# Performance work log

Hardware: AMD Instinct MI355X
Metric: run time of the kernel (lower is better)

Reference implementation:

```python
import jax, jax.numpy as jnp
import numpy as np

B, C, T = 8, 256, 2048
REDUCED = max(C // 8, 8)  # 32


def setup_inputs() -> dict:
    key = jax.random.key(0)
    ks = jax.random.split(key, 7)
    s = 1.0 / np.sqrt(C)
    return {
        "x": jax.random.normal(ks[0], (B, C, T), dtype=jnp.float32),
        "Wq": jax.random.uniform(ks[1], (REDUCED, C), jnp.float32, -s, s),
        "bq": jax.random.uniform(ks[2], (REDUCED,), jnp.float32, -s, s),
        "Wk": jax.random.uniform(ks[3], (REDUCED, C), jnp.float32, -s, s),
        "bk": jax.random.uniform(ks[4], (REDUCED,), jnp.float32, -s, s),
        "Wv": jax.random.uniform(ks[5], (C, C), jnp.float32, -s, s),
        "bv": jax.random.uniform(ks[6], (C,), jnp.float32, -s, s),
        "gamma": jnp.zeros((1,), dtype=jnp.float32) + 0.1,  # nonzero so output depends on attention
    }


def reference(x, Wq, bq, Wk, bk, Wv, bv, gamma):
    # conv1x1 projections == per-timestep linear over channels
    q = jnp.einsum("rc,bct->btr", Wq, x) + bq            # [B, T, reduced]
    k = jnp.einsum("rc,bct->brt", Wk, x) + bk[:, None]   # [B, reduced, T]
    v = jnp.einsum("oc,bct->bto", Wv, x) + bv            # [B, T, C]
    attn = jnp.einsum("btr,brs->bts", q, k)              # [B, T, T]
    attn = jax.nn.softmax(attn, axis=-1)
    out = jnp.einsum("bts,bsc->btc", attn, v)            # [B, T, C]
    out = jnp.transpose(out, (0, 2, 1))                  # [B, C, T]
    return x + gamma * out
```

## Files before the change

### kernel.cpp

```cpp
#include <hip/hip_runtime.h>
#include <hip/hip_bf16.h>
#include <math.h>

constexpr int BB = 8;
constexpr int CC = 256;
constexpr int TT = 2048;
constexpr int RR = 32;

constexpr int ATILE = 64;
constexpr int PS = 72;

constexpr int PT  = 32;
constexpr int XS32 = 33;
constexpr int XSB  = 264;

constexpr float FIXEDM = 24.0f;

typedef short short8 __attribute__((ext_vector_type(8)));
typedef float f32x4 __attribute__((ext_vector_type(4)));
typedef unsigned short us4 __attribute__((ext_vector_type(4)));

static __device__ __forceinline__ unsigned short f2bf(float f) {
    __hip_bfloat16 h = __float2bfloat16(f);
    return *reinterpret_cast<unsigned short*>(&h);
}

__global__ __launch_bounds__(256) void wcast_kernel(
    const float* __restrict__ Wq, const float* __restrict__ Wk,
    const float* __restrict__ Wv,
    unsigned short* __restrict__ wqb, unsigned short* __restrict__ wkb,
    unsigned short* __restrict__ wvb)
{
    int g = blockIdx.x * 256 + threadIdx.x;
    const float* src; unsigned short* dst; int i4;
    if (g < 2048)       { src = Wq; dst = wqb; i4 = g; }
    else if (g < 4096)  { src = Wk; dst = wkb; i4 = g - 2048; }
    else                { src = Wv; dst = wvb; i4 = g - 4096; }
    float4 v = *(const float4*)(src + i4 * 4);
    us4 p;
    p[0] = f2bf(v.x); p[1] = f2bf(v.y); p[2] = f2bf(v.z); p[3] = f2bf(v.w);
    *(us4*)(dst + i4 * 4) = p;
}

__global__ __launch_bounds__(256, 2) void proj_kernel(
    const float* __restrict__ x,
    const unsigned short* __restrict__ wqb, const float* __restrict__ bq,
    const unsigned short* __restrict__ wkb, const float* __restrict__ bk,
    const unsigned short* __restrict__ wvb, const float* __restrict__ bv,
    unsigned short* __restrict__ qws, unsigned short* __restrict__ kws,
    unsigned short* __restrict__ vws)
{
    __shared__ float xs32[CC * XS32];
    __shared__ unsigned short xsb[PT * XSB];

    const int tid = threadIdx.x;
    const int t0  = blockIdx.x * PT;
    const int b   = blockIdx.y;
    const float* xb = x + (size_t)b * CC * TT;

    #pragma unroll
    for (int m = 0; m < 8; ++m) {
        int lin = m * 256 + tid;
        int c   = lin >> 3;
        int t4  = lin & 7;
        float4 v = *(const float4*)(xb + (size_t)c * TT + t0 + t4 * 4);
        float* d = &xs32[c * XS32 + t4 * 4];
        d[0] = v.x; d[1] = v.y; d[2] = v.z; d[3] = v.w;
    }
    __syncthreads();
    {
        int c = tid;
        #pragma unroll
        for (int t = 0; t < PT; ++t)
            xsb[t * XSB + c] = f2bf(xs32[c * XS32 + t]);
    }
    __syncthreads();

    const int lane = tid & 63;
    const int w    = __builtin_amdgcn_readfirstlane(tid >> 6);
    const int l15  = lane & 15;
    const int quad = lane >> 4;

    const unsigned short* Wt[5]; const float* bt[5]; int rl[5]; int seg[5];
    #pragma unroll
    for (int i = 0; i < 5; ++i) {
        int mt = w * 5 + i;
        if (mt < 2)      { Wt[i] = wqb; bt[i] = bq; rl[i] = mt * 16;       seg[i] = 0; }
        else if (mt < 4) { Wt[i] = wkb; bt[i] = bk; rl[i] = (mt - 2) * 16; seg[i] = 1; }
        else             { Wt[i] = wvb; bt[i] = bv; rl[i] = (mt - 4) * 16; seg[i] = 2; }
    }

    f32x4 acc[5][2];
    #pragma unroll
    for (int i = 0; i < 5; ++i) {
        float4 bb = *(const float4*)(bt[i] + rl[i] + quad * 4);
        #pragma unroll
        for (int nt = 0; nt < 2; ++nt)
            acc[i][nt] = (f32x4){bb.x, bb.y, bb.z, bb.w};
    }

    #pragma unroll
    for (int ks = 0; ks < 8; ++ks) {
        short8 bfr[2];
        #pragma unroll
        for (int nt = 0; nt < 2; ++nt)
            bfr[nt] = *(const short8*)(&xsb[(nt * 16 + l15) * XSB + ks * 32 + quad * 8]);
        #pragma unroll
        for (int i = 0; i < 5; ++i) {
            short8 af = *(const short8*)(Wt[i] + (size_t)(rl[i] + l15) * CC + ks * 32 + quad * 8);
            #pragma unroll
            for (int nt = 0; nt < 2; ++nt)
                acc[i][nt] = __builtin_amdgcn_mfma_f32_16x16x32_bf16(
                    af, bfr[nt], acc[i][nt], 0, 0, 0);
        }
    }

    #pragma unroll
    for (int i = 0; i < 5; ++i) {
        if (seg[i] < 2) {
            unsigned short* outt = (seg[i] == 0 ? qws : kws) + (size_t)b * TT * RR;
            #pragma unroll
            for (int nt = 0; nt < 2; ++nt) {
                int t = t0 + nt * 16 + l15;
                us4 pk;
                pk[0] = f2bf(acc[i][nt][0]); pk[1] = f2bf(acc[i][nt][1]);
                pk[2] = f2bf(acc[i][nt][2]); pk[3] = f2bf(acc[i][nt][3]);
                *(us4*)(outt + (size_t)t * RR + rl[i] + quad * 4) = pk;
            }
        } else {
            unsigned short* vt = vws + (size_t)b * CC * TT;
            #pragma unroll
            for (int nt = 0; nt < 2; ++nt)
                #pragma unroll
                for (int r = 0; r < 4; ++r)
                    vt[(size_t)(rl[i] + quad * 4 + r) * TT + t0 + nt * 16 + l15] =
                        f2bf(acc[i][nt][r]);
        }
    }
}

__global__ __launch_bounds__(512, 2) void attn_kernel(
    const float* __restrict__ x,
    const unsigned short* __restrict__ qws, const unsigned short* __restrict__ kws,
    const unsigned short* __restrict__ vws, const float* __restrict__ gamma_p,
    float* __restrict__ out)
{
    __shared__ unsigned short Vs[2][CC * 64];
    __shared__ unsigned short Ps[2][ATILE * PS];
    __shared__ float lsum[2][ATILE];

    const int tid  = threadIdx.x;
    const int b    = blockIdx.x;
    const int t0   = blockIdx.y * ATILE;
    const int lane = tid & 63;
    const int w    = __builtin_amdgcn_readfirstlane(tid >> 6);
    const int mt_s = w & 3;
    const int sh_w = w >> 2;
    const int mth  = w >> 2;
    const int cq   = w & 3;
    const int l15  = lane & 15;
    const int quad = lane >> 4;

    const unsigned short* qb = qws + (size_t)b * TT * RR;
    const unsigned short* kb = kws + (size_t)b * TT * RR;
    const unsigned short* vb = vws + (size_t)b * CC * TT;

    short8 qfrag = *(const short8*)(qb + (size_t)(t0 + mt_s * 16 + l15) * RR + quad * 8);

    const int crow = tid >> 3;
    const int sg   = (tid & 7) ^ (crow & 7);
    const unsigned short* vstg = vb + (size_t)crow * TT + sg * 8;

    const unsigned short* kbase = kb + (size_t)(sh_w * 32 + l15) * RR + quad * 8;

    float rs[4];
    #pragma unroll
    for (int r = 0; r < 4; ++r) rs[r] = 0.0f;

    f32x4 acc[2][4];
    #pragma unroll
    for (int mt = 0; mt < 2; ++mt)
        #pragma unroll
        for (int nt = 0; nt < 4; ++nt)
            acc[mt][nt] = (f32x4){0.f, 0.f, 0.f, 0.f};

    const f32x4 zz = (f32x4){0.f, 0.f, 0.f, 0.f};

    short8 vreg[4], kcur[2], kn[2];

    #pragma unroll
    for (int m = 0; m < 4; ++m)
        vreg[m] = *(const short8*)(vstg + (size_t)(m * 64) * TT);
    #pragma unroll
    for (int i = 0; i < 2; ++i)
        kcur[i] = *(const short8*)(kbase + (size_t)(i * 16) * RR);
    #pragma unroll
    for (int m = 0; m < 4; ++m)
        *(short8*)(&Vs[0][(m * 512 + tid) * 8]) = vreg[m];

    #pragma unroll 2
    for (int j = 0; j < 32; ++j) {
        const int s1 = ((j + 1) & 31) * 64;
        #pragma unroll
        for (int m = 0; m < 4; ++m)
            vreg[m] = *(const short8*)(vstg + (size_t)(m * 64) * TT + s1);
        #pragma unroll
        for (int i = 0; i < 2; ++i)
            kn[i] = *(const short8*)(kbase + (size_t)(s1 + i * 16) * RR);

        f32x4 st[2];
        #pragma unroll
        for (int i = 0; i < 2; ++i)
            st[i] = __builtin_amdgcn_mfma_f32_16x16x32_bf16(qfrag, kcur[i], zz, 0, 0, 0);

        const int prow = mt_s * 16 + quad * 4;
        const int scol = sh_w * 32;
        #pragma unroll
        for (int i = 0; i < 2; ++i) {
            #pragma unroll
            for (int r = 0; r < 4; ++r) {
                float e = __expf(st[i][r] - FIXEDM);
                rs[r] += e;
                Ps[j & 1][(prow + r) * PS + scol + i * 16 + l15] = f2bf(e);
            }
        }
        __syncthreads();

        #pragma unroll
        for (int ks = 0; ks < 2; ++ks) {
            short8 pa[2], vf[4];
            #pragma unroll
            for (int mt = 0; mt < 2; ++mt)
                pa[mt] = *(const short8*)(&Ps[j & 1][(mth * 32 + mt * 16 + l15) * PS + ks * 32 + quad * 8]);
            #pragma unroll
            for (int nt = 0; nt < 4; ++nt) {
                int c = cq * 64 + nt * 16 + l15;
                int o16 = c * 8 + ((ks * 4 + quad) ^ (l15 & 7));
                vf[nt] = *(const short8*)(&Vs[j & 1][o16 * 8]);
            }
            #pragma unroll
            for (int mt = 0; mt < 2; ++mt)
                #pragma unroll
                for (int nt = 0; nt < 4; ++nt)
                    acc[mt][nt] = __builtin_amdgcn_mfma_f32_16x16x32_bf16(
                        pa[mt], vf[nt], acc[mt][nt], 0, 0, 0);
        }

        #pragma unroll
        for (int m = 0; m < 4; ++m)
            *(short8*)(&Vs[(j + 1) & 1][(m * 512 + tid) * 8]) = vreg[m];

        #pragma unroll
        for (int i = 0; i < 2; ++i) kcur[i] = kn[i];
    }

    #pragma unroll
    for (int mask = 1; mask < 16; mask <<= 1)
        #pragma unroll
        for (int r = 0; r < 4; ++r)
            rs[r] += __shfl_xor(rs[r], mask, 64);
    if (l15 == 0) {
        #pragma unroll
        for (int r = 0; r < 4; ++r)
            lsum[sh_w][mt_s * 16 + quad * 4 + r] = rs[r];
    }
    __syncthreads();

    const float gam = gamma_p[0];
    const float* xb = x + (size_t)b * CC * TT;
    float* ob = out + (size_t)b * CC * TT;

    #pragma unroll
    for (int mt = 0; mt < 2; ++mt) {
        int tbase = mth * 32 + mt * 16 + quad * 4;
        f32x4 l0 = *(const f32x4*)(&lsum[0][tbase]);
        f32x4 l1 = *(const f32x4*)(&lsum[1][tbase]);
        float li[4];
        #pragma unroll
        for (int r = 0; r < 4; ++r) li[r] = 1.0f / (l0[r] + l1[r]);
        #pragma unroll
        for (int nt = 0; nt < 4; ++nt) {
            int c = cq * 64 + nt * 16 + l15;
            size_t gidx = (size_t)c * TT + t0 + tbase;
            float4 xv = *(const float4*)(xb + gidx);
            float4 ov;
            ov.x = xv.x + gam * acc[mt][nt][0] * li[0];
            ov.y = xv.y + gam * acc[mt][nt][1] * li[1];
            ov.z = xv.z + gam * acc[mt][nt][2] * li[2];
            ov.w = xv.w + gam * acc[mt][nt][3] * li[3];
            *(float4*)(ob + gidx) = ov;
        }
    }
}

extern "C" void kernel_launch(void* const* d_in, const int* in_sizes, int n_in,
                              void* d_out, int out_size, void* d_ws, size_t ws_size,
                              hipStream_t stream)
{
    const float* x     = (const float*)d_in[0];
    const float* Wq    = (const float*)d_in[1];
    const float* bq    = (const float*)d_in[2];
    const float* Wk    = (const float*)d_in[3];
    const float* bk    = (const float*)d_in[4];
    const float* Wv    = (const float*)d_in[5];
    const float* bv    = (const float*)d_in[6];
    const float* gamma = (const float*)d_in[7];
    float* out = (float*)d_out;

    unsigned short* qws = (unsigned short*)d_ws;
    unsigned short* kws = qws + (size_t)BB * TT * RR;
    unsigned short* vws = kws + (size_t)BB * TT * RR;
    unsigned short* wqb = vws + (size_t)BB * CC * TT;
    unsigned short* wkb = wqb + (size_t)RR * CC;
    unsigned short* wvb = wkb + (size_t)RR * CC;

    wcast_kernel<<<80, 256, 0, stream>>>(Wq, Wk, Wv, wqb, wkb, wvb);

    dim3 pgrid(TT / PT, BB);
    proj_kernel<<<pgrid, 256, 0, stream>>>(x, wqb, bq, wkb, bk, wvb, bv, qws, kws, vws);

    dim3 agrid(BB, TT / ATILE);
    attn_kernel<<<agrid, 512, 0, stream>>>(x, qws, kws, vws, gamma, out);
}
```

Measured before the change: 129.4 us.

## Warp-specialize attention kernel into producer and consumer wave groups

Splits the 8 waves into 4 producer waves and 4 consumer waves. The producers load V into LDS, compute QK scores, exponentiate them, and write P one tile ahead. The consumers run the P·V MFMAs on the previous tile and write the output epilogue. The aim is to overlap the global loads and exp work with matrix math so each tile needs one barrier instead of a serialized phase. In exchange, the consumers hold more accumulator registers (4x4 tiles), and only half the waves issue MFMAs, which risks leaving the matrix units underused.

```diff
diff --git a/kernel.cpp b/kernel.cpp
--- a/kernel.cpp
+++ b/kernel.cpp
@@ -147,17 +147,13 @@
 {
     __shared__ unsigned short Vs[2][CC * 64];
     __shared__ unsigned short Ps[2][ATILE * PS];
-    __shared__ float lsum[2][ATILE];
+    __shared__ float lsum[ATILE];
 
     const int tid  = threadIdx.x;
     const int b    = blockIdx.x;
     const int t0   = blockIdx.y * ATILE;
     const int lane = tid & 63;
     const int w    = __builtin_amdgcn_readfirstlane(tid >> 6);
-    const int mt_s = w & 3;
-    const int sh_w = w >> 2;
-    const int mth  = w >> 2;
-    const int cq   = w & 3;
     const int l15  = lane & 15;
     const int quad = lane >> 4;
 
@@ -165,130 +161,160 @@
     const unsigned short* kb = kws + (size_t)b * TT * RR;
     const unsigned short* vb = vws + (size_t)b * CC * TT;
 
-    short8 qfrag = *(const short8*)(qb + (size_t)(t0 + mt_s * 16 + l15) * RR + quad * 8);
-
-    const int crow = tid >> 3;
-    const int sg   = (tid & 7) ^ (crow & 7);
-    const unsigned short* vstg = vb + (size_t)crow * TT + sg * 8;
-
-    const unsigned short* kbase = kb + (size_t)(sh_w * 32 + l15) * RR + quad * 8;
-
-    float rs[4];
-    #pragma unroll
-    for (int r = 0; r < 4; ++r) rs[r] = 0.0f;
-
-    f32x4 acc[2][4];
-    #pragma unroll
-    for (int mt = 0; mt < 2; ++mt)
-        #pragma unroll
-        for (int nt = 0; nt < 4; ++nt)
-            acc[mt][nt] = (f32x4){0.f, 0.f, 0.f, 0.f};
-
-    const f32x4 zz = (f32x4){0.f, 0.f, 0.f, 0.f};
-
-    short8 vreg[4], kcur[2], kn[2];
-
-    #pragma unroll
-    for (int m = 0; m < 4; ++m)
-        vreg[m] = *(const short8*)(vstg + (size_t)(m * 64) * TT);
-    #pragma unroll
-    for (int i = 0; i < 2; ++i)
-        kcur[i] = *(const short8*)(kbase + (size_t)(i * 16) * RR);
-    #pragma unroll
-    for (int m = 0; m < 4; ++m)
-        *(short8*)(&Vs[0][(m * 512 + tid) * 8]) = vreg[m];
-
-    #pragma unroll 2
-    for (int j = 0; j < 32; ++j) {
-        const int s1 = ((j + 1) & 31) * 64;
-        #pragma unroll
-        for (int m = 0; m < 4; ++m)
-            vreg[m] = *(const short8*)(vstg + (size_t)(m * 64) * TT + s1);
-        #pragma unroll
-        for (int i = 0; i < 2; ++i)
-            kn[i] = *(const short8*)(kbase + (size_t)(s1 + i * 16) * RR);
-
-        f32x4 st[2];
-        #pragma unroll
-        for (int i = 0; i < 2; ++i)
-            st[i] = __builtin_amdgcn_mfma_f32_16x16x32_bf16(qfrag, kcur[i], zz, 0, 0, 0);
-
-        const int prow = mt_s * 16 + quad * 4;
-        const int scol = sh_w * 32;
-        #pragma unroll
-        for (int i = 0; i < 2; ++i) {
-            #pragma unroll
-            for (int r = 0; r < 4; ++r) {
-                float e = __expf(st[i][r] - FIXEDM);
-                rs[r] += e;
-                Ps[j & 1][(prow + r) * PS + scol + i * 16 + l15] = f2bf(e);
-            }
-        }
-        __syncthreads();
-
-        #pragma unroll
-        for (int ks = 0; ks < 2; ++ks) {
-            short8 pa[2], vf[4];
-            #pragma unroll
-            for (int mt = 0; mt < 2; ++mt)
-                pa[mt] = *(const short8*)(&Ps[j & 1][(mth * 32 + mt * 16 + l15) * PS + ks * 32 + quad * 8]);
-            #pragma unroll
-            for (int nt = 0; nt < 4; ++nt) {
-                int c = cq * 64 + nt * 16 + l15;
-                int o16 = c * 8 + ((ks * 4 + quad) ^ (l15 & 7));
-                vf[nt] = *(const short8*)(&Vs[j & 1][o16 * 8]);
-            }
-            #pragma unroll
-            for (int mt = 0; mt < 2; ++mt)
-                #pragma unroll
-                for (int nt = 0; nt < 4; ++nt)
-                    acc[mt][nt] = __builtin_amdgcn_mfma_f32_16x16x32_bf16(
-                        pa[mt], vf[nt], acc[mt][nt], 0, 0, 0);
-        }
-
-        #pragma unroll
-        for (int m = 0; m < 4; ++m)
-            *(short8*)(&Vs[(j + 1) & 1][(m * 512 + tid) * 8]) = vreg[m];
-
-        #pragma unroll
-        for (int i = 0; i < 2; ++i) kcur[i] = kn[i];
-    }
-
-    #pragma unroll
-    for (int mask = 1; mask < 16; mask <<= 1)
-        #pragma unroll
-        for (int r = 0; r < 4; ++r)
-            rs[r] += __shfl_xor(rs[r], mask, 64);
-    if (l15 == 0) {
-        #pragma unroll
-        for (int r = 0; r < 4; ++r)
-            lsum[sh_w][mt_s * 16 + quad * 4 + r] = rs[r];
-    }
-    __syncthreads();
-
     const float gam = gamma_p[0];
     const float* xb = x + (size_t)b * CC * TT;
     float* ob = out + (size_t)b * CC * TT;
 
-    #pragma unroll
-    for (int mt = 0; mt < 2; ++mt) {
-        int tbase = mth * 32 + mt * 16 + quad * 4;
-        f32x4 l0 = *(const f32x4*)(&lsum[0][tbase]);
-        f32x4 l1 = *(const f32x4*)(&lsum[1][tbase]);
-        float li[4];
-        #pragma unroll
-        for (int r = 0; r < 4; ++r) li[r] = 1.0f / (l0[r] + l1[r]);
-        #pragma unroll
-        for (int nt = 0; nt < 4; ++nt) {
-            int c = cq * 64 + nt * 16 + l15;
-            size_t gidx = (size_t)c * TT + t0 + tbase;
-            float4 xv = *(const float4*)(xb + gidx);
-            float4 ov;
-            ov.x = xv.x + gam * acc[mt][nt][0] * li[0];
-            ov.y = xv.y + gam * acc[mt][nt][1] * li[1];
-            ov.z = xv.z + gam * acc[mt][nt][2] * li[2];
-            ov.w = xv.w + gam * acc[mt][nt][3] * li[3];
-            *(float4*)(ob + gidx) = ov;
+    if (w < 4) {
+        const int p    = w;
+        const int ptid = tid & 255;
+
+        short8 qfrag = *(const short8*)(qb + (size_t)(t0 + p * 16 + l15) * RR + quad * 8);
+
+        const int crow = ptid >> 3;
+        const int sg0  = (ptid & 7);
+        const unsigned short* vstg[8];
+        #pragma unroll
+        for (int m = 0; m < 8; ++m) {
+            int c  = m * 32 + crow;
+            int sg = sg0 ^ (c & 7);
+            vstg[m] = vb + (size_t)c * TT + sg * 8;
+        }
+        const unsigned short* kbase = kb + (size_t)l15 * RR + quad * 8;
+
+        float rs[4];
+        #pragma unroll
+        for (int r = 0; r < 4; ++r) rs[r] = 0.0f;
+
+        short8 vreg[8], kcur[4];
+
+        #pragma unroll
+        for (int m = 0; m < 8; ++m)
+            vreg[m] = *(const short8*)(vstg[m]);
+        #pragma unroll
+        for (int i = 0; i < 4; ++i)
+            kcur[i] = *(const short8*)(kbase + (size_t)(i * 16) * RR);
+        #pragma unroll
+        for (int m = 0; m < 8; ++m)
+            *(short8*)(&Vs[0][(m * 256 + ptid) * 8]) = vreg[m];
+        {
+            const f32x4 zz = (f32x4){0.f, 0.f, 0.f, 0.f};
+            const int prow = p * 16 + quad * 4;
+            #pragma unroll
+            for (int nt = 0; nt < 4; ++nt) {
+                f32x4 st = __builtin_amdgcn_mfma_f32_16x16x32_bf16(qfrag, kcur[nt], zz, 0, 0, 0);
+                #pragma unroll
+                for (int r = 0; r < 4; ++r) {
+                    float e = __expf(st[r] - FIXEDM);
+                    rs[r] += e;
+                    Ps[0][(prow + r) * PS + nt * 16 + l15] = f2bf(e);
+                }
+            }
+        }
+        #pragma unroll
+        for (int m = 0; m < 8; ++m)
+            vreg[m] = *(const short8*)(vstg[m] + 64);
+        #pragma unroll
+        for (int i = 0; i < 4; ++i)
+            kcur[i] = *(const short8*)(kbase + (size_t)(64 + i * 16) * RR);
+
+        #pragma unroll 2
+        for (int j = 0; j < 32; ++j) {
+            __syncthreads();
+            if (j < 31) {
+                #pragma unroll
+                for (int m = 0; m < 8; ++m)
+                    *(short8*)(&Vs[(j + 1) & 1][(m * 256 + ptid) * 8]) = vreg[m];
+                const f32x4 zz = (f32x4){0.f, 0.f, 0.f, 0.f};
+                const int prow = p * 16 + quad * 4;
+                #pragma unroll
+                for (int nt = 0; nt < 4; ++nt) {
+                    f32x4 st = __builtin_amdgcn_mfma_f32_16x16x32_bf16(qfrag, kcur[nt], zz, 0, 0, 0);
+                    #pragma unroll
+                    for (int r = 0; r < 4; ++r) {
+                        float e = __expf(st[r] - FIXEDM);
+                        rs[r] += e;
+                        Ps[(j + 1) & 1][(prow + r) * PS + nt * 16 + l15] = f2bf(e);
+                    }
+                }
+                if (j < 30) {
+                    const int s2 = (j + 2) * 64;
+                    #pragma unroll
+                    for (int m = 0; m < 8; ++m)
+                        vreg[m] = *(const short8*)(vstg[m] + s2);
+                    #pragma unroll
+                    for (int i = 0; i < 4; ++i)
+                        kcur[i] = *(const short8*)(kbase + (size_t)(s2 + i * 16) * RR);
+                }
+            }
+        }
+
+        #pragma unroll
+        for (int mask = 1; mask < 16; mask <<= 1)
+            #pragma unroll
+            for (int r = 0; r < 4; ++r)
+                rs[r] += __shfl_xor(rs[r], mask, 64);
+        if (l15 == 0) {
+            #pragma unroll
+            for (int r = 0; r < 4; ++r)
+                lsum[p * 16 + quad * 4 + r] = rs[r];
+        }
+        __syncthreads();
+    } else {
+        const int cq = w - 4;
+
+        f32x4 acc[4][4];
+        #pragma unroll
+        for (int mt = 0; mt < 4; ++mt)
+            #pragma unroll
+            for (int nt = 0; nt < 4; ++nt)
+                acc[mt][nt] = (f32x4){0.f, 0.f, 0.f, 0.f};
+
+        #pragma unroll 2
+        for (int j = 0; j < 32; ++j) {
+            __syncthreads();
+            const int par = j & 1;
+            #pragma unroll
+            for (int ks = 0; ks < 2; ++ks) {
+                short8 pa[4], vf[4];
+                #pragma unroll
+                for (int mt = 0; mt < 4; ++mt)
+                    pa[mt] = *(const short8*)(&Ps[par][(mt * 16 + l15) * PS + ks * 32 + quad * 8]);
+                #pragma unroll
+                for (int nt = 0; nt < 4; ++nt) {
+                    int c = cq * 64 + nt * 16 + l15;
+                    int o16 = c * 8 + ((ks * 4 + quad) ^ (l15 & 7));
+                    vf[nt] = *(const short8*)(&Vs[par][o16 * 8]);
+                }
+                #pragma unroll
+                for (int mt = 0; mt < 4; ++mt)
+                    #pragma unroll
+                    for (int nt = 0; nt < 4; ++nt)
+                        acc[mt][nt] = __builtin_amdgcn_mfma_f32_16x16x32_bf16(
+                            pa[mt], vf[nt], acc[mt][nt], 0, 0, 0);
+            }
+        }
+        __syncthreads();
+
+        #pragma unroll
+        for (int mt = 0; mt < 4; ++mt) {
+            int tbase = mt * 16 + quad * 4;
+            f32x4 lv = *(const f32x4*)(&lsum[tbase]);
+            float li[4];
+            #pragma unroll
+            for (int r = 0; r < 4; ++r) li[r] = 1.0f / lv[r];
+            #pragma unroll
+            for (int nt = 0; nt < 4; ++nt) {
+                int c = cq * 64 + nt * 16 + l15;
+                size_t gidx = (size_t)c * TT + t0 + tbase;
+                float4 xv = *(const float4*)(xb + gidx);
+                float4 ov;
+                ov.x = xv.x + gam * acc[mt][nt][0] * li[0];
+                ov.y = xv.y + gam * acc[mt][nt][1] * li[1];
+                ov.z = xv.z + gam * acc[mt][nt][2] * li[2];
+                ov.w = xv.w + gam * acc[mt][nt][3] * li[3];
+                *(float4*)(ob + gidx) = ov;
+            }
         }
     }
 }
```

New measurement: 140.8 us. +8.7%, slower.

## Move x transpose and bf16 cast into prep kernel, read MFMA operands from global

Applied to the files above, without the earlier changes.

The fp32-to-bf16 cast and transpose of x move out of the projection kernel into the weight-cast kernel, which now writes a bf16 [B,T,C] copy of x to workspace. The projection kernel drops its 33 KB fp32 and bf16 shared-memory staging and both barriers, loading MFMA B fragments directly from the transposed global buffer. This is meant to cut LDS use and raise occupancy in the projection stage. In exchange it adds an extra global write and read of x in bf16, and the prep kernel now has 592 blocks instead of 80.

```diff
diff --git a/kernel.cpp b/kernel.cpp
--- a/kernel.cpp
+++ b/kernel.cpp
@@ -12,7 +12,6 @@
 
 constexpr int PT  = 32;
 constexpr int XS32 = 33;
-constexpr int XSB  = 264;
 
 constexpr float FIXEDM = 24.0f;
 
@@ -25,37 +24,33 @@
     return *reinterpret_cast<unsigned short*>(&h);
 }
 
-__global__ __launch_bounds__(256) void wcast_kernel(
+__global__ __launch_bounds__(256) void xprep_kernel(
+    const float* __restrict__ x, unsigned short* __restrict__ xT,
     const float* __restrict__ Wq, const float* __restrict__ Wk,
     const float* __restrict__ Wv,
     unsigned short* __restrict__ wqb, unsigned short* __restrict__ wkb,
     unsigned short* __restrict__ wvb)
 {
-    int g = blockIdx.x * 256 + threadIdx.x;
-    const float* src; unsigned short* dst; int i4;
-    if (g < 2048)       { src = Wq; dst = wqb; i4 = g; }
-    else if (g < 4096)  { src = Wk; dst = wkb; i4 = g - 2048; }
-    else                { src = Wv; dst = wvb; i4 = g - 4096; }
-    float4 v = *(const float4*)(src + i4 * 4);
-    us4 p;
-    p[0] = f2bf(v.x); p[1] = f2bf(v.y); p[2] = f2bf(v.z); p[3] = f2bf(v.w);
-    *(us4*)(dst + i4 * 4) = p;
-}
-
-__global__ __launch_bounds__(256, 2) void proj_kernel(
-    const float* __restrict__ x,
-    const unsigned short* __restrict__ wqb, const float* __restrict__ bq,
-    const unsigned short* __restrict__ wkb, const float* __restrict__ bk,
-    const unsigned short* __restrict__ wvb, const float* __restrict__ bv,
-    unsigned short* __restrict__ qws, unsigned short* __restrict__ kws,
-    unsigned short* __restrict__ vws)
-{
+    const int tid = threadIdx.x;
+
+    if (blockIdx.x >= 512) {
+        int g = (blockIdx.x - 512) * 256 + tid;
+        const float* src; unsigned short* dst; int i4;
+        if (g < 2048)       { src = Wq; dst = wqb; i4 = g; }
+        else if (g < 4096)  { src = Wk; dst = wkb; i4 = g - 2048; }
+        else                { src = Wv; dst = wvb; i4 = g - 4096; }
+        float4 v = *(const float4*)(src + i4 * 4);
+        us4 p;
+        p[0] = f2bf(v.x); p[1] = f2bf(v.y); p[2] = f2bf(v.z); p[3] = f2bf(v.w);
+        *(us4*)(dst + i4 * 4) = p;
+        return;
+    }
+
     __shared__ float xs32[CC * XS32];
-    __shared__ unsigned short xsb[PT * XSB];
-
-    const int tid = threadIdx.x;
-    const int t0  = blockIdx.x * PT;
-    const int b   = blockIdx.y;
+
+    const int tile = blockIdx.x & 63;
+    const int b    = blockIdx.x >> 6;
+    const int t0   = tile * PT;
     const float* xb = x + (size_t)b * CC * TT;
 
     #pragma unroll
@@ -68,13 +63,32 @@
         d[0] = v.x; d[1] = v.y; d[2] = v.z; d[3] = v.w;
     }
     __syncthreads();
-    {
-        int c = tid;
-        #pragma unroll
-        for (int t = 0; t < PT; ++t)
-            xsb[t * XSB + c] = f2bf(xs32[c * XS32 + t]);
-    }
-    __syncthreads();
+
+    const int trow = tid >> 3;
+    const int oct  = tid & 7;
+    unsigned short* xrow = xT + ((size_t)b * TT + t0 + trow) * CC;
+    #pragma unroll
+    for (int it = 0; it < 4; ++it) {
+        int c0 = it * 64 + oct * 8;
+        short8 pk;
+        #pragma unroll
+        for (int j = 0; j < 8; ++j)
+            pk[j] = (short)f2bf(xs32[(c0 + j) * XS32 + trow]);
+        *(short8*)(xrow + c0) = pk;
+    }
+}
+
+__global__ __launch_bounds__(256, 2) void proj_kernel(
+    const unsigned short* __restrict__ xT,
+    const unsigned short* __restrict__ wqb, const float* __restrict__ bq,
+    const unsigned short* __restrict__ wkb, const float* __restrict__ bk,
+    const unsigned short* __restrict__ wvb, const float* __restrict__ bv,
+    unsigned short* __restrict__ qws, unsigned short* __restrict__ kws,
+    unsigned short* __restrict__ vws)
+{
+    const int tid = threadIdx.x;
+    const int t0  = blockIdx.x * PT;
+    const int b   = blockIdx.y;
 
     const int lane = tid & 63;
     const int w    = __builtin_amdgcn_readfirstlane(tid >> 6);
@@ -90,6 +104,13 @@
         else             { Wt[i] = wvb; bt[i] = bv; rl[i] = (mt - 4) * 16; seg[i] = 2; }
     }
 
+    const unsigned short* xr0 = xT + ((size_t)b * TT + t0 + l15) * CC + quad * 8;
+    const unsigned short* xr1 = xr0 + (size_t)16 * CC;
+    const unsigned short* wr[5];
+    #pragma unroll
+    for (int i = 0; i < 5; ++i)
+        wr[i] = Wt[i] + (size_t)(rl[i] + l15) * CC + quad * 8;
+
     f32x4 acc[5][2];
     #pragma unroll
     for (int i = 0; i < 5; ++i) {
@@ -101,17 +122,13 @@
 
     #pragma unroll
     for (int ks = 0; ks < 8; ++ks) {
-        short8 bfr[2];
-        #pragma unroll
-        for (int nt = 0; nt < 2; ++nt)
-            bfr[nt] = *(const short8*)(&xsb[(nt * 16 + l15) * XSB + ks * 32 + quad * 8]);
+        short8 bfr0 = *(const short8*)(xr0 + ks * 32);
+        short8 bfr1 = *(const short8*)(xr1 + ks * 32);
         #pragma unroll
         for (int i = 0; i < 5; ++i) {
-            short8 af = *(const short8*)(Wt[i] + (size_t)(rl[i] + l15) * CC + ks * 32 + quad * 8);
-            #pragma unroll
-            for (int nt = 0; nt < 2; ++nt)
-                acc[i][nt] = __builtin_amdgcn_mfma_f32_16x16x32_bf16(
-                    af, bfr[nt], acc[i][nt], 0, 0, 0);
+            short8 af = *(const short8*)(wr[i] + ks * 32);
+            acc[i][0] = __builtin_amdgcn_mfma_f32_16x16x32_bf16(af, bfr0, acc[i][0], 0, 0, 0);
+            acc[i][1] = __builtin_amdgcn_mfma_f32_16x16x32_bf16(af, bfr1, acc[i][1], 0, 0, 0);
         }
     }
 
@@ -313,11 +330,12 @@
     unsigned short* wqb = vws + (size_t)BB * CC * TT;
     unsigned short* wkb = wqb + (size_t)RR * CC;
     unsigned short* wvb = wkb + (size_t)RR * CC;
-
-    wcast_kernel<<<80, 256, 0, stream>>>(Wq, Wk, Wv, wqb, wkb, wvb);
+    unsigned short* xT  = wvb + (size_t)CC * CC;
+
+    xprep_kernel<<<592, 256, 0, stream>>>(x, xT, Wq, Wk, Wv, wqb, wkb, wvb);
 
     dim3 pgrid(TT / PT, BB);
-    proj_kernel<<<pgrid, 256, 0, stream>>>(x, wqb, bq, wkb, bk, wvb, bv, qws, kws, vws);
+    proj_kernel<<<pgrid, 256, 0, stream>>>(xT, wqb, bq, wkb, bk, wvb, bv, qws, kws, vws);
 
     dim3 agrid(BB, TT / ATILE);
     attn_kernel<<<agrid, 512, 0, stream>>>(x, qws, kws, vws, gamma, out);
```

Result: slower. 132.4 us (+2.3%).
